# Performance work log

Hardware: AMD Instinct MI355X
Metric: run time of the kernel (lower is better)

Reference implementation:

```python
import jax, jax.numpy as jnp
import numpy as np

S, R, CM, H, CA, CZ = 128, 256, 256, 8, 32, 128


def _ln(x, w, b):
    mu = x.mean(-1, keepdims=True)
    var = x.var(-1, keepdims=True)
    return (x - mu) * jax.lax.rsqrt(var + 1e-5) * w + b


def setup_inputs() -> dict:
    key = jax.random.key(0)
    ks = jax.random.split(key, 20)
    n = lambda i, shape: jax.random.normal(ks[i], shape, jnp.float32) * 0.05
    return {
        "m": jax.random.normal(ks[0], (S, R, CM), jnp.float32),
        "m_mask": jnp.ones((S, R), jnp.float32),
        "z": jax.random.normal(ks[1], (R, R, CZ), jnp.float32),
        "row_ln_w": jnp.ones((CM,)), "row_ln_b": jnp.zeros((CM,)),
        "row_z_ln_w": jnp.ones((CZ,)), "row_z_ln_b": jnp.zeros((CZ,)),
        "row_wq": n(2, (CM, H * CA)), "row_wk": n(3, (CM, H * CA)), "row_wv": n(4, (CM, H * CA)),
        "row_wb": n(5, (CZ, H)),
        "row_wg": n(6, (CM, H * CA)), "row_bg": jnp.zeros((H * CA,)),
        "row_wo": n(7, (H * CA, CM)), "row_bo": jnp.zeros((CM,)),
        "col_ln_w": jnp.ones((CM,)), "col_ln_b": jnp.zeros((CM,)),
        "col_wq": n(8, (CM, H * CA)), "col_wk": n(9, (CM, H * CA)), "col_wv": n(10, (CM, H * CA)),
        "col_wg": n(11, (CM, H * CA)), "col_bg": jnp.zeros((H * CA,)),
        "col_wo": n(12, (H * CA, CM)), "col_bo": jnp.zeros((CM,)),
        "tr_ln_w": jnp.ones((CM,)), "tr_ln_b": jnp.zeros((CM,)),
        "tr_w1": n(13, (CM, 4 * CM)), "tr_b1": jnp.zeros((4 * CM,)),
        "tr_w2": n(14, (4 * CM, CM)), "tr_b2": jnp.zeros((CM,)),
    }


def _row_atten(m, m_mask, z, ln_w, ln_b, z_ln_w, z_ln_b, wq, wk, wv, wb, wg, bg, wo, bo):
    # MSA row attention with pair bias: attend over residues within each sequence row.
    x = _ln(m, ln_w, ln_b)                                   # [s,r,cm]
    q = (x @ wq).reshape(S, R, H, CA) * (CA ** -0.5)
    k = (x @ wk).reshape(S, R, H, CA)
    v = (x @ wv).reshape(S, R, H, CA)
    pair_bias = jnp.transpose(_ln(z, z_ln_w, z_ln_b) @ wb, (2, 0, 1))  # [h,r,r]
    mask_bias = (m_mask - 1.0)[:, None, None, :] * 1e9       # [s,1,1,r] over keys
    logits = jnp.einsum('sqhc,skhc->shqk', q, k) + pair_bias[None] + mask_bias
    a = jax.nn.softmax(logits, axis=-1)
    o = jnp.einsum('shqk,skhc->sqhc', a, v)
    g = jax.nn.sigmoid(x @ wg + bg).reshape(S, R, H, CA)
    return (g * o).reshape(S, R, H * CA) @ wo + bo


def _col_atten(m, m_mask, ln_w, ln_b, wq, wk, wv, wg, bg, wo, bo):
    # MSA column attention: attend over sequences within each residue column.
    x = _ln(m, ln_w, ln_b)                                   # [s,r,cm]
    q = (x @ wq).reshape(S, R, H, CA) * (CA ** -0.5)
    k = (x @ wk).reshape(S, R, H, CA)
    v = (x @ wv).reshape(S, R, H, CA)
    mask_bias = (jnp.transpose(m_mask) - 1.0)[:, None, None, :] * 1e9  # [r,1,1,s]
    logits = jnp.einsum('qrhc,krhc->rhqk', q, k) + mask_bias
    a = jax.nn.softmax(logits, axis=-1)
    o = jnp.einsum('rhqk,krhc->qrhc', a, v)
    g = jax.nn.sigmoid(x @ wg + bg).reshape(S, R, H, CA)
    return (g * o).reshape(S, R, H * CA) @ wo + bo


def _transition(m, ln_w, ln_b, w1, b1, w2, b2):
    x = _ln(m, ln_w, ln_b)
    return jax.nn.relu(x @ w1 + b1) @ w2 + b2


def reference(m, m_mask, z,
              row_ln_w, row_ln_b, row_z_ln_w, row_z_ln_b,
              row_wq, row_wk, row_wv, row_wb, row_wg, row_bg, row_wo, row_bo,
              col_ln_w, col_ln_b, col_wq, col_wk, col_wv, col_wg, col_bg, col_wo, col_bo,
              tr_ln_w, tr_ln_b, tr_w1, tr_b1, tr_w2, tr_b2):
    m = m + _row_atten(m, m_mask, z, row_ln_w, row_ln_b, row_z_ln_w, row_z_ln_b,
                       row_wq, row_wk, row_wv, row_wb, row_wg, row_bg, row_wo, row_bo)
    m = m + _col_atten(m, m_mask, col_ln_w, col_ln_b, col_wq, col_wk, col_wv,
                       col_wg, col_bg, col_wo, col_bo)
    m = m + _transition(m, tr_ln_w, tr_ln_b, tr_w1, tr_b1, tr_w2, tr_b2)
    return m
```

## Files before the change

### kernel.cpp

```cpp
#include <hip/hip_runtime.h>
#include <stdint.h>

#define S_ 128
#define R_ 256
#define CM_ 256
#define H_ 8
#define CA_ 32
#define CZ_ 128

typedef unsigned short u16;
typedef __bf16 bf16x8 __attribute__((ext_vector_type(8)));
typedef float f32x4 __attribute__((ext_vector_type(4)));

#define LOG2E 1.4426950408889634f

__device__ __forceinline__ float bf2f(u16 u){ unsigned v = ((unsigned)u) << 16; float f; __builtin_memcpy(&f, &v, 4); return f; }
__device__ __forceinline__ u16 f2bf(float f){ __bf16 h = (__bf16)f; u16 u; __builtin_memcpy(&u, &h, 2); return u; }
__device__ __forceinline__ unsigned pkbf(float lo, float hi){
  unsigned r; asm("v_cvt_pk_bf16_f32 %0, %1, %2" : "=v"(r) : "v"(lo), "v"(hi)); return r;
}
__device__ __forceinline__ float fexp2(float x){
  float r; asm("v_exp_f32 %0, %1" : "=v"(r) : "v"(x)); return r;
}

__device__ __forceinline__ void gl16(const void* g, void* l){
  __builtin_amdgcn_global_load_lds((const __attribute__((address_space(1))) void*)g,
                                   (__attribute__((address_space(3))) void*)l, 16, 0, 0);
}

struct WSrc { const float* p[12]; };
__global__ __launch_bounds__(256) void transpose_all(WSrc srcs, u16* __restrict__ dst){
  int b = blockIdx.x, t = threadIdx.x;
  int job, idx;
  if(b < 2560){ job = b >> 8; idx = ((b & 255) << 8) + t; }
  else if(b < 3584){ job = 10; idx = ((b - 2560) << 8) + t; }
  else { job = 11; idx = ((b - 3584) << 8) + t; }
  int K = (job == 11) ? 1024 : 256;
  int N = (job == 10) ? 1024 : 256;
  int off;
  if(job < 10) off = job * 65536;
  else if(job == 10) off = 655360;
  else off = 917504;
  int k = idx / N, n = idx - k * N;
  float sc = (job == 0 || job == 5) ? (0.17677669529663687f * LOG2E) : 1.f;
  dst[off + n * K + k] = f2bf(srcs.p[job][idx] * sc);
}

template<bool BF16IN>
__global__ __launch_bounds__(256) void ln_kernel(const void* __restrict__ inv, const float* __restrict__ w,
                          const float* __restrict__ b, u16* __restrict__ out){
  int wv = threadIdx.x >> 6, lane = threadIdx.x & 63;
  long long row = (long long)blockIdx.x * 4 + wv;
  float vx, vy, vz, vw;
  if(BF16IN){
    ushort4 v4 = ((const ushort4*)((const u16*)inv + row * CM_))[lane];
    vx = bf2f(v4.x); vy = bf2f(v4.y); vz = bf2f(v4.z); vw = bf2f(v4.w);
  } else {
    float4 v4 = ((const float4*)((const float*)inv + row * CM_))[lane];
    vx = v4.x; vy = v4.y; vz = v4.z; vw = v4.w;
  }
  float s = vx + vy + vz + vw;
  for(int mo = 32; mo; mo >>= 1) s += __shfl_xor(s, mo, 64);
  float mu = s * (1.f / CM_);
  float dx = vx - mu, dy = vy - mu, dz = vz - mu, dw = vw - mu;
  float s2 = dx * dx + dy * dy + dz * dz + dw * dw;
  for(int mo = 32; mo; mo >>= 1) s2 += __shfl_xor(s2, mo, 64);
  float rstd = rsqrtf(s2 * (1.f / CM_) + 1e-5f);
  float4 w4 = ((const float4*)w)[lane];
  float4 b4 = ((const float4*)b)[lane];
  ushort4 st;
  st.x = f2bf(dx * rstd * w4.x + b4.x);
  st.y = f2bf(dy * rstd * w4.y + b4.y);
  st.z = f2bf(dz * rstd * w4.z + b4.z);
  st.w = f2bf(dw * rstd * w4.w + b4.w);
  *(ushort4*)(out + row * CM_ + lane * 4) = st;
}

__global__ __launch_bounds__(256) void pair_bias_kernel(const float* __restrict__ z, const float* __restrict__ lnw,
                                 const float* __restrict__ lnb, const float* __restrict__ wb,
                                 u16* __restrict__ pb){
  __shared__ __attribute__((aligned(16))) unsigned char Xl[32 * 256];
  __shared__ __attribute__((aligned(16))) unsigned char Wl[16 * 256];
  const int t = threadIdx.x;
  const int wv = t >> 6, lane = t & 63, l15 = lane & 15, l4 = lane >> 4;
  const int r0 = blockIdx.x * 32;

  if(t < 128){
    const float4* wr = (const float4*)(wb + t * 8);
    float4 a = wr[0], bq = wr[1];
    u16 vals[8] = {f2bf(a.x), f2bf(a.y), f2bf(a.z), f2bf(a.w),
                   f2bf(bq.x), f2bf(bq.y), f2bf(bq.z), f2bf(bq.w)};
    #pragma unroll
    for(int n = 0; n < 8; n++){
      *(u16*)(Wl + ((n * 256 + t * 2) ^ ((n & 7) << 4))) = vals[n];
      *(u16*)(Wl + (((n + 8) * 256 + t * 2) ^ ((n & 7) << 4))) = 0;
    }
  }
  {
    int row = wv * 8 + (lane >> 3);
    int c0 = (lane & 7) * 16;
    const float4* rp = (const float4*)(z + (long long)(r0 + row) * CZ_ + c0);
    float4 v0 = rp[0], v1 = rp[1], v2 = rp[2], v3 = rp[3];
    float s = v0.x + v0.y + v0.z + v0.w + v1.x + v1.y + v1.z + v1.w
            + v2.x + v2.y + v2.z + v2.w + v3.x + v3.y + v3.z + v3.w;
    s += __shfl_xor(s, 1, 64); s += __shfl_xor(s, 2, 64); s += __shfl_xor(s, 4, 64);
    float mu = s * (1.f / CZ_);
    float d[16] = {v0.x - mu, v0.y - mu, v0.z - mu, v0.w - mu,
                   v1.x - mu, v1.y - mu, v1.z - mu, v1.w - mu,
                   v2.x - mu, v2.y - mu, v2.z - mu, v2.w - mu,
                   v3.x - mu, v3.y - mu, v3.z - mu, v3.w - mu};
    float s2 = 0.f;
    #pragma unroll
    for(int i = 0; i < 16; i++) s2 += d[i] * d[i];
    s2 += __shfl_xor(s2, 1, 64); s2 += __shfl_xor(s2, 2, 64); s2 += __shfl_xor(s2, 4, 64);
    float rstd = rsqrtf(s2 * (1.f / CZ_) + 1e-5f);
    const float4* wp = (const float4*)(lnw + c0);
    const float4* bp = (const float4*)(lnb + c0);
    float x[16];
    #pragma unroll
    for(int i = 0; i < 4; i++){
      float4 w4 = wp[i], b4 = bp[i];
      x[i * 4 + 0] = d[i * 4 + 0] * rstd * w4.x + b4.x;
      x[i * 4 + 1] = d[i * 4 + 1] * rstd * w4.y + b4.y;
      x[i * 4 + 2] = d[i * 4 + 2] * rstd * w4.z + b4.z;
      x[i * 4 + 3] = d[i * 4 + 3] * rstd * w4.w + b4.w;
    }
    uint4 p0, p1;
    p0.x = pkbf(x[0], x[1]);  p0.y = pkbf(x[2], x[3]);
    p0.z = pkbf(x[4], x[5]);  p0.w = pkbf(x[6], x[7]);
    p1.x = pkbf(x[8], x[9]);  p1.y = pkbf(x[10], x[11]);
    p1.z = pkbf(x[12], x[13]); p1.w = pkbf(x[14], x[15]);
    *(uint4*)(Xl + ((row * 256 + c0 * 2) ^ ((row & 7) << 4))) = p0;
    *(uint4*)(Xl + ((row * 256 + c0 * 2 + 16) ^ ((row & 7) << 4))) = p1;
  }
  __syncthreads();
  if(wv < 2){
    f32x4 acc = {0.f, 0.f, 0.f, 0.f};
    #pragma unroll
    for(int ks = 0; ks < 4; ks++){
      int rowA = wv * 16 + l15;
      bf16x8 a = *(const bf16x8*)(Xl + ((rowA * 256 + l4 * 16 + ks * 64) ^ ((rowA & 7) << 4)));
      bf16x8 b = *(const bf16x8*)(Wl + ((l15 * 256 + l4 * 16 + ks * 64) ^ ((l15 & 7) << 4)));
      acc = __builtin_amdgcn_mfma_f32_16x16x32_bf16(a, b, acc, 0, 0, 0);
    }
    if(l15 < 8){
      #pragma unroll
      for(int r = 0; r < 4; r++){
        int rowg = r0 + wv * 16 + l4 * 4 + r;
        int q = rowg >> 8, k = rowg & 255;
        int off = (((l15 * 16 + (q >> 4)) * 16 + (k >> 4)) << 10)
                + ((((q >> 2) & 3) * 16 + (k & 15)) << 2) + (q & 3);
        pb[off] = f2bf(acc[r] * LOG2E);
      }
    }
  }
}

template<bool HAS_BIAS, bool HAS_SIG, bool RELU, int RESMODE, bool F32OUT>
__global__ __launch_bounds__(256) void gemm128(
    const u16* __restrict__ A, const u16* __restrict__ Wt,
    const float* __restrict__ bias, const void* __restrict__ res,
    void* __restrict__ outv, int M, int N, int K, int sigStart){
  __shared__ __attribute__((aligned(16))) unsigned char Ab[16384];
  __shared__ __attribute__((aligned(16))) unsigned char Bb[16384];
  const int t = threadIdx.x;
  const int wv = t >> 6, lane = t & 63, l15 = lane & 15, l4 = lane >> 4;
  const int wm = wv >> 1, wn = wv & 1;
  const unsigned flat = blockIdx.y * gridDim.x + blockIdx.x;
  const unsigned NB = gridDim.x, mper = gridDim.y >> 3;
  const unsigned xcd = flat & 7, j = flat >> 3;
  const unsigned n_blk = j % NB, m_blk = xcd * mper + j / NB;
  const long long m0 = (long long)m_blk * 128;
  const int n0 = n_blk * 128;
  const int srow = t >> 3;
  const int ksw  = ((t & 7) ^ (srow & 7)) * 8;
  const u16* Ag = A  + (m0 + srow) * (long long)K + ksw;
  const u16* Bg = Wt + (long long)(n0 + srow) * K + ksw;
  f32x4 acc[4][4] = {};
  for(int kk = 0; kk < K; kk += 64){
    #pragma unroll
    for(int i = 0; i < 4; i++){
      gl16(Ag + (long long)i * 32 * K + kk, Ab + wv * 1024 + lane * 16 + i * 4096);
      gl16(Bg + (long long)i * 32 * K + kk, Bb + wv * 1024 + lane * 16 + i * 4096);
    }
    asm volatile("s_waitcnt vmcnt(0)" ::: "memory");
    __syncthreads();
    #pragma unroll
    for(int kh = 0; kh < 2; kh++){
      bf16x8 af[4], bq[4];
      #pragma unroll
      for(int mt = 0; mt < 4; mt++){
        int rr = wm * 64 + mt * 16 + l15;
        af[mt] = *(const bf16x8*)(Ab + rr * 128 + ((kh * 64 + l4 * 16) ^ ((rr & 7) << 4)));
      }
      #pragma unroll
      for(int nt = 0; nt < 4; nt++){
        int rr = wn * 64 + nt * 16 + l15;
        bq[nt] = *(const bf16x8*)(Bb + rr * 128 + ((kh * 64 + l4 * 16) ^ ((rr & 7) << 4)));
      }
      #pragma unroll
      for(int mt = 0; mt < 4; mt++)
        #pragma unroll
        for(int nt = 0; nt < 4; nt++)
          acc[mt][nt] = __builtin_amdgcn_mfma_f32_16x16x32_bf16(af[mt], bq[nt], acc[mt][nt], 0, 0, 0);
    }
    __syncthreads();
  }
  float bnt[4]; bool sg[4];
  #pragma unroll
  for(int nt = 0; nt < 4; nt++){
    int ncol = n0 + wn * 64 + nt * 16 + l15;
    bnt[nt] = 0.f; sg[nt] = false;
    if(HAS_BIAS){
      if(HAS_SIG){ sg[nt] = (ncol >= sigStart); bnt[nt] = sg[nt] ? bias[ncol - sigStart] : 0.f; }
      else bnt[nt] = bias[ncol];
    }
  }
  #pragma unroll
  for(int mt = 0; mt < 4; mt++){
    #pragma unroll
    for(int r = 0; r < 4; r++){
      long long mrow = m0 + wm * 64 + mt * 16 + l4 * 4 + r;
      #pragma unroll
      for(int nt = 0; nt < 4; nt++){
        int ncol = n0 + wn * 64 + nt * 16 + l15;
        float v = acc[mt][nt][r] + bnt[nt];
        if(HAS_SIG){ if(sg[nt]) v = 1.f / (1.f + __expf(-v)); }
        if(RELU) v = v > 0.f ? v : 0.f;
        if(RESMODE == 1) v += ((const float*)res)[mrow * N + ncol];
        if(RESMODE == 2) v += bf2f(((const u16*)res)[mrow * N + ncol]);
        if(F32OUT) ((float*)outv)[mrow * N + ncol] = v;
        else       ((u16*)outv)[mrow * N + ncol] = f2bf(v);
      }
    }
  }
}

template<int L, int SPLIT, bool HAS_BIAS>
__global__ __launch_bounds__(256) void atten_kernel(
    const u16* __restrict__ qg, const u16* __restrict__ kg, const u16* __restrict__ vg,
    const u16* __restrict__ gg, const u16* __restrict__ pb, const float* __restrict__ mask,
    u16* __restrict__ og,
    long long obase_mul, long long tstride, long long obase_o, long long ostride,
    long long mbase_mul, int mstride){
  __shared__ __attribute__((aligned(16))) unsigned char smem[L * 128 + 8192];
  unsigned char* Kl = smem;
  unsigned char* Vt = smem + L * 64;
  unsigned char* Pl = smem + L * 128;

  const int t = threadIdx.x;
  const int wv = t >> 6, lane = t & 63, l15 = lane & 15, l4 = lane >> 4;
  const int h = blockIdx.x & 7;
  const int g2 = blockIdx.x >> 3;
  const int sp = g2 % SPLIT;
  const int outer = g2 / SPLIT;
  const long long base  = (long long)outer * obase_mul + h * CA_;
  const long long baseo = (long long)outer * obase_o  + h * CA_;
  const long long mb = (long long)outer * mbase_mul;
  const int KT = L / 16, NC = L / 64, QB = L / SPLIT;

  #pragma unroll
  for(int j = 0; j < L * 4; j += 256){
    int cid = j + t;
    int row = cid >> 2, ko = cid & 3;
    int4 kv = *(const int4*)(kg + base + (long long)row * tstride + ko * 8);
    *(int4*)(Kl + ((row * 64 + ko * 16) ^ ((row & 7) << 4))) = kv;
  }
  if(t < L){
    __attribute__((aligned(16))) u16 tmp[32];
    const u16* vp = vg + base + (long long)t * tstride;
    #pragma unroll
    for(int j2 = 0; j2 < 4; j2++) ((int4*)tmp)[j2] = *(const int4*)(vp + j2 * 8);
    int kp = (t >> 6) * 64 + (t & 15) * 4 + ((t >> 4) & 3);
    #pragma unroll
    for(int c = 0; c < 32; c++)
      *(u16*)(Vt + (((c * L + kp) * 2) ^ ((c & 7) << 4))) = tmp[c];
  }
  __syncthreads();

  float mskb[L / 16];
  #pragma unroll
  for(int kt = 0; kt < KT; kt++)
    mskb[kt] = (mask[mb + (long long)(kt * 16 + l15) * mstride] - 1.f) * (1e9f * LOG2E);

  unsigned char* Pw = Pl + wv * 2048;
  #pragma unroll
  for(int qt = 0; qt < QB / 64; qt++){
    const int qrow0 = sp * QB + wv * (QB / 4) + qt * 16;
    bf16x8 aq = *(const bf16x8*)(qg + base + (long long)(qrow0 + l15) * tstride + l4 * 8);
    f32x4 lac[L / 16];
    #pragma unroll
    for(int kt = 0; kt < KT; kt++){
      int kr = kt * 16 + l15;
      bf16x8 bk = *(const bf16x8*)(Kl + ((kr * 64 + l4 * 16) ^ ((kr & 7) << 4)));
      f32x4 zz = {0.f, 0.f, 0.f, 0.f};
      lac[kt] = __builtin_amdgcn_mfma_f32_16x16x32_bf16(aq, bk, zz, 0, 0, 0);
    }
    const u16* tile = HAS_BIAS ? (pb + (((h * 16 + (qrow0 >> 4)) * 16) << 10) + lane * 4) : nullptr;
    float sm[4] = {1e-30f, 1e-30f, 1e-30f, 1e-30f};
    #pragma unroll
    for(int kt = 0; kt < KT; kt++){
      float mm = mskb[kt];
      if(HAS_BIAS){
        ushort4 b4 = *(const ushort4*)(tile + (kt << 10));
        lac[kt][0] = fexp2(lac[kt][0] + mm + bf2f(b4.x));
        lac[kt][1] = fexp2(lac[kt][1] + mm + bf2f(b4.y));
        lac[kt][2] = fexp2(lac[kt][2] + mm + bf2f(b4.z));
        lac[kt][3] = fexp2(lac[kt][3] + mm + bf2f(b4.w));
      } else {
        #pragma unroll
        for(int r = 0; r < 4; r++) lac[kt][r] = fexp2(lac[kt][r] + mm);
      }
      #pragma unroll
      for(int r = 0; r < 4; r++) sm[r] += lac[kt][r];
    }
    #pragma unroll
    for(int mo = 1; mo < 16; mo <<= 1)
      #pragma unroll
      for(int r = 0; r < 4; r++) sm[r] += __shfl_xor(sm[r], mo, 64);
    float inv[4];
    #pragma unroll
    for(int r = 0; r < 4; r++) inv[r] = 1.f / sm[r];
    f32x4 oac[2] = {{0,0,0,0},{0,0,0,0}};
    #pragma unroll
    for(int ch = 0; ch < NC; ch++){
      asm volatile("" ::: "memory");
      #pragma unroll
      for(int r = 0; r < 4; r++){
        int qp = l4 * 4 + r;
        uint2 pk2;
        pk2.x = pkbf(lac[ch * 4 + 0][r], lac[ch * 4 + 1][r]);
        pk2.y = pkbf(lac[ch * 4 + 2][r], lac[ch * 4 + 3][r]);
        *(uint2*)(Pw + qp * 128 + ((l15 * 8) ^ ((qp & 7) << 4))) = pk2;
      }
      asm volatile("s_waitcnt lgkmcnt(0)" ::: "memory");
      #pragma unroll
      for(int ksl = 0; ksl < 2; ksl++){
        bf16x8 ap = *(const bf16x8*)(Pw + l15 * 128 + ((ksl * 64 + l4 * 16) ^ ((l15 & 7) << 4)));
        #pragma unroll
        for(int ct = 0; ct < 2; ct++){
          int c = ct * 16 + l15;
          bf16x8 bv = *(const bf16x8*)(Vt + (((c * L + ch * 64 + ksl * 32 + l4 * 8) * 2) ^ ((c & 7) << 4)));
          oac[ct] = __builtin_amdgcn_mfma_f32_16x16x32_bf16(ap, bv, oac[ct], 0, 0, 0);
        }
      }
    }
    #pragma unroll
    for(int ct = 0; ct < 2; ct++)
      #pragma unroll
      for(int r = 0; r < 4; r++){
        int qi = qrow0 + l4 * 4 + r, c = ct * 16 + l15;
        float g = bf2f(gg[base + (long long)qi * tstride + c]);
        og[baseo + (long long)qi * ostride + c] = f2bf(oac[ct][r] * inv[r] * g);
      }
  }
}

extern "C" void kernel_launch(void* const* d_in, const int* in_sizes, int n_in,
                              void* d_out, int out_size, void* d_ws, size_t ws_size,
                              hipStream_t stream){
  const float* m        = (const float*)d_in[0];
  const float* m_mask   = (const float*)d_in[1];
  const float* z        = (const float*)d_in[2];
  const float* row_ln_w = (const float*)d_in[3];
  const float* row_ln_b = (const float*)d_in[4];
  const float* row_z_ln_w = (const float*)d_in[5];
  const float* row_z_ln_b = (const float*)d_in[6];
  const float* row_bg   = (const float*)d_in[12];
  const float* row_bo   = (const float*)d_in[14];
  const float* col_ln_w = (const float*)d_in[15];
  const float* col_ln_b = (const float*)d_in[16];
  const float* col_bg   = (const float*)d_in[21];
  const float* col_bo   = (const float*)d_in[23];
  const float* tr_ln_w  = (const float*)d_in[24];
  const float* tr_ln_b  = (const float*)d_in[25];
  const float* tr_b1    = (const float*)d_in[27];
  const float* tr_b2    = (const float*)d_in[29];
  float* out = (float*)d_out;
  char* ws = (char*)d_ws;

  u16* bx  = (u16*)ws;
  u16* fq  = bx + 8388608;
  u16* t_o = fq + 33554432;
  u16* pb  = t_o + 8388608;
  u16* wt  = pb + 2097152;
  u16* m2  = fq;
  u16* h1  = fq + 8388608;

  WSrc srcs;
  srcs.p[0] = (const float*)d_in[7];
  srcs.p[1] = (const float*)d_in[8];
  srcs.p[2] = (const float*)d_in[9];
  srcs.p[3] = (const float*)d_in[11];
  srcs.p[4] = (const float*)d_in[13];
  srcs.p[5] = (const float*)d_in[17];
  srcs.p[6] = (const float*)d_in[18];
  srcs.p[7] = (const float*)d_in[19];
  srcs.p[8] = (const float*)d_in[20];
  srcs.p[9] = (const float*)d_in[22];
  srcs.p[10] = (const float*)d_in[26];
  srcs.p[11] = (const float*)d_in[28];

  dim3 b256(256);
  transpose_all<<<dim3(4608), b256, 0, stream>>>(srcs, wt);
  pair_bias_kernel<<<dim3(2048), b256, 0, stream>>>(z, row_z_ln_w, row_z_ln_b,
                                                    (const float*)d_in[10], pb);

  ln_kernel<false><<<dim3(8192), b256, 0, stream>>>(m, row_ln_w, row_ln_b, bx);
  gemm128<true,true,false,0,false><<<dim3(8,256), b256, 0, stream>>>(
      bx, wt, row_bg, nullptr, fq, 32768, 1024, 256, 768);
  atten_kernel<256,2,true><<<dim3(2048), b256, 0, stream>>>(
      fq, fq + 256, fq + 512, fq + 768, pb, m_mask, t_o,
      262144, 1024, 65536, 256, 256, 1);
  gemm128<true,false,false,1,false><<<dim3(2,256), b256, 0, stream>>>(
      t_o, wt + 262144, row_bo, m, bx, 32768, 256, 256, 0);

  ln_kernel<true><<<dim3(8192), b256, 0, stream>>>(bx, col_ln_w, col_ln_b, t_o);
  gemm128<true,true,false,0,false><<<dim3(8,256), b256, 0, stream>>>(
      t_o, wt + 327680, col_bg, nullptr, fq, 32768, 1024, 256, 768);
  atten_kernel<128,2,false><<<dim3(4096), b256, 0, stream>>>(
      fq, fq + 256, fq + 512, fq + 768, nullptr, m_mask, t_o,
      1024, 262144, 256, 65536, 1, 256);
  gemm128<true,false,false,2,false><<<dim3(2,256), b256, 0, stream>>>(
      t_o, wt + 589824, col_bo, bx, m2, 32768, 256, 256, 0);

  ln_kernel<true><<<dim3(8192), b256, 0, stream>>>(m2, tr_ln_w, tr_ln_b, bx);
  gemm128<true,false,true,0,false><<<dim3(8,256), b256, 0, stream>>>(
      bx, wt + 655360, tr_b1, nullptr, h1, 32768, 1024, 256, 0);
  gemm128<true,false,false,2,true><<<dim3(2,256), b256, 0, stream>>>(
      h1, wt + 917504, tr_b2, m2, out, 32768, 256, 1024, 0);
}
```

Before: 283.5 us.

## Write QKVG projections head-major so attention reads contiguous per-head tiles

The QKV+gate GEMM epilogue now scatters its output into a head-major layout ([section][token][32]). For column attention it also transposes the token order so each column's rows are contiguous. The attention kernel then loads K, V, Q and gate with a fixed 64-byte row stride instead of a 2 KB stride, which should improve coalescing and cache-line use. The kernel also drops the query split, so each block handles all queries of a row or column with half as many blocks. Costs are scattered 64-byte writes in the GEMM epilogue and fewer, longer-running attention blocks.

```diff
diff --git a/kernel.cpp b/kernel.cpp
--- a/kernel.cpp
+++ b/kernel.cpp
@@ -156,7 +156,7 @@
   }
 }
 
-template<bool HAS_BIAS, bool HAS_SIG, bool RELU, int RESMODE, bool F32OUT>
+template<bool HAS_BIAS, bool HAS_SIG, bool RELU, int RESMODE, bool F32OUT, int OUTMODE>
 __global__ __launch_bounds__(256) void gemm128(
     const u16* __restrict__ A, const u16* __restrict__ Wt,
     const float* __restrict__ bias, const void* __restrict__ res,
@@ -221,6 +221,8 @@
     #pragma unroll
     for(int r = 0; r < 4; r++){
       long long mrow = m0 + wm * 64 + mt * 16 + l4 * 4 + r;
+      long long tok = mrow;
+      if(OUTMODE == 2) tok = (((mrow & 255) << 7) | (mrow >> 8));
       #pragma unroll
       for(int nt = 0; nt < 4; nt++){
         int ncol = n0 + wn * 64 + nt * 16 + l15;
@@ -229,19 +231,22 @@
         if(RELU) v = v > 0.f ? v : 0.f;
         if(RESMODE == 1) v += ((const float*)res)[mrow * N + ncol];
         if(RESMODE == 2) v += bf2f(((const u16*)res)[mrow * N + ncol]);
-        if(F32OUT) ((float*)outv)[mrow * N + ncol] = v;
-        else       ((u16*)outv)[mrow * N + ncol] = f2bf(v);
-      }
-    }
-  }
-}
-
-template<int L, int SPLIT, bool HAS_BIAS>
+        long long oidx;
+        if(OUTMODE == 0) oidx = mrow * N + ncol;
+        else oidx = ((long long)(ncol >> 5) << 20) + tok * 32 + (ncol & 31);
+        if(F32OUT) ((float*)outv)[oidx] = v;
+        else       ((u16*)outv)[oidx] = f2bf(v);
+      }
+    }
+  }
+}
+
+template<int L, bool HAS_BIAS>
 __global__ __launch_bounds__(256) void atten_kernel(
     const u16* __restrict__ qg, const u16* __restrict__ kg, const u16* __restrict__ vg,
     const u16* __restrict__ gg, const u16* __restrict__ pb, const float* __restrict__ mask,
     u16* __restrict__ og,
-    long long obase_mul, long long tstride, long long obase_o, long long ostride,
+    long long obase_in, long long obase_o, long long ostride,
     long long mbase_mul, int mstride){
   __shared__ __attribute__((aligned(16))) unsigned char smem[L * 128 + 8192];
   unsigned char* Kl = smem;
@@ -251,24 +256,22 @@
   const int t = threadIdx.x;
   const int wv = t >> 6, lane = t & 63, l15 = lane & 15, l4 = lane >> 4;
   const int h = blockIdx.x & 7;
-  const int g2 = blockIdx.x >> 3;
-  const int sp = g2 % SPLIT;
-  const int outer = g2 / SPLIT;
-  const long long base  = (long long)outer * obase_mul + h * CA_;
-  const long long baseo = (long long)outer * obase_o  + h * CA_;
+  const int outer = blockIdx.x >> 3;
+  const long long base  = ((long long)h << 20) + (long long)outer * obase_in;
+  const long long baseo = (long long)outer * obase_o + h * CA_;
   const long long mb = (long long)outer * mbase_mul;
-  const int KT = L / 16, NC = L / 64, QB = L / SPLIT;
+  const int KT = L / 16, NC = L / 64;
 
   #pragma unroll
   for(int j = 0; j < L * 4; j += 256){
     int cid = j + t;
     int row = cid >> 2, ko = cid & 3;
-    int4 kv = *(const int4*)(kg + base + (long long)row * tstride + ko * 8);
+    int4 kv = *(const int4*)(kg + base + row * 32 + ko * 8);
     *(int4*)(Kl + ((row * 64 + ko * 16) ^ ((row & 7) << 4))) = kv;
   }
   if(t < L){
     __attribute__((aligned(16))) u16 tmp[32];
-    const u16* vp = vg + base + (long long)t * tstride;
+    const u16* vp = vg + base + t * 32;
     #pragma unroll
     for(int j2 = 0; j2 < 4; j2++) ((int4*)tmp)[j2] = *(const int4*)(vp + j2 * 8);
     int kp = (t >> 6) * 64 + (t & 15) * 4 + ((t >> 4) & 3);
@@ -284,10 +287,11 @@
     mskb[kt] = (mask[mb + (long long)(kt * 16 + l15) * mstride] - 1.f) * (1e9f * LOG2E);
 
   unsigned char* Pw = Pl + wv * 2048;
+  const int NQ = L / 4;
   #pragma unroll
-  for(int qt = 0; qt < QB / 64; qt++){
-    const int qrow0 = sp * QB + wv * (QB / 4) + qt * 16;
-    bf16x8 aq = *(const bf16x8*)(qg + base + (long long)(qrow0 + l15) * tstride + l4 * 8);
+  for(int qt = 0; qt < NQ / 16; qt++){
+    const int qrow0 = wv * NQ + qt * 16;
+    bf16x8 aq = *(const bf16x8*)(qg + base + (qrow0 + l15) * 32 + l4 * 8);
     f32x4 lac[L / 16];
     #pragma unroll
     for(int kt = 0; kt < KT; kt++){
@@ -350,7 +354,7 @@
       #pragma unroll
       for(int r = 0; r < 4; r++){
         int qi = qrow0 + l4 * 4 + r, c = ct * 16 + l15;
-        float g = bf2f(gg[base + (long long)qi * tstride + c]);
+        float g = bf2f(gg[base + qi * 32 + c]);
         og[baseo + (long long)qi * ostride + c] = f2bf(oac[ct][r] * inv[r] * g);
       }
   }
@@ -387,6 +391,8 @@
   u16* m2  = fq;
   u16* h1  = fq + 8388608;
 
+  const long long HSEC = 1ll << 20;
+
   WSrc srcs;
   srcs.p[0] = (const float*)d_in[7];
   srcs.p[1] = (const float*)d_in[8];
@@ -407,26 +413,26 @@
                                                     (const float*)d_in[10], pb);
 
   ln_kernel<false><<<dim3(8192), b256, 0, stream>>>(m, row_ln_w, row_ln_b, bx);
-  gemm128<true,true,false,0,false><<<dim3(8,256), b256, 0, stream>>>(
+  gemm128<true,true,false,0,false,1><<<dim3(8,256), b256, 0, stream>>>(
       bx, wt, row_bg, nullptr, fq, 32768, 1024, 256, 768);
-  atten_kernel<256,2,true><<<dim3(2048), b256, 0, stream>>>(
-      fq, fq + 256, fq + 512, fq + 768, pb, m_mask, t_o,
-      262144, 1024, 65536, 256, 256, 1);
-  gemm128<true,false,false,1,false><<<dim3(2,256), b256, 0, stream>>>(
+  atten_kernel<256,true><<<dim3(1024), b256, 0, stream>>>(
+      fq, fq + 8 * HSEC, fq + 16 * HSEC, fq + 24 * HSEC, pb, m_mask, t_o,
+      8192, 65536, 256, 256, 1);
+  gemm128<true,false,false,1,false,0><<<dim3(2,256), b256, 0, stream>>>(
       t_o, wt + 262144, row_bo, m, bx, 32768, 256, 256, 0);
 
   ln_kernel<true><<<dim3(8192), b256, 0, stream>>>(bx, col_ln_w, col_ln_b, t_o);
-  gemm128<true,true,false,0,false><<<dim3(8,256), b256, 0, stream>>>(
+  gemm128<true,true,false,0,false,2><<<dim3(8,256), b256, 0, stream>>>(
       t_o, wt + 327680, col_bg, nullptr, fq, 32768, 1024, 256, 768);
-  atten_kernel<128,2,false><<<dim3(4096), b256, 0, stream>>>(
-      fq, fq + 256, fq + 512, fq + 768, nullptr, m_mask, t_o,
-      1024, 262144, 256, 65536, 1, 256);
-  gemm128<true,false,false,2,false><<<dim3(2,256), b256, 0, stream>>>(
+  atten_kernel<128,false><<<dim3(2048), b256, 0, stream>>>(
+      fq, fq + 8 * HSEC, fq + 16 * HSEC, fq + 24 * HSEC, nullptr, m_mask, t_o,
+      4096, 256, 65536, 1, 256);
+  gemm128<true,false,false,2,false,0><<<dim3(2,256), b256, 0, stream>>>(
       t_o, wt + 589824, col_bo, bx, m2, 32768, 256, 256, 0);
 
   ln_kernel<true><<<dim3(8192), b256, 0, stream>>>(m2, tr_ln_w, tr_ln_b, bx);
-  gemm128<true,false,true,0,false><<<dim3(8,256), b256, 0, stream>>>(
+  gemm128<true,false,true,0,false,0><<<dim3(8,256), b256, 0, stream>>>(
       bx, wt + 655360, tr_b1, nullptr, h1, 32768, 1024, 256, 0);
-  gemm128<true,false,false,2,true><<<dim3(2,256), b256, 0, stream>>>(
+  gemm128<true,false,false,2,true,0><<<dim3(2,256), b256, 0, stream>>>(
       h1, wt + 917504, tr_b2, m2, out, 32768, 256, 1024, 0);
 }
```

Measured after the change: 268.2 us. 1.06x faster.
